# Optimization experiments

Hardware: AMD Instinct MI355X
Metric: run time of the kernel (lower is better)

## Reference

```python
import jax, jax.numpy as jnp
import numpy as np

B, D, H = 4096, 32, 1024  # batch, in_out_dim, hidden width


def setup_inputs() -> dict:
    key = jax.random.key(0)
    ks = jax.random.split(key, 10)

    def lin_w(k, shape, fan_in):
        bound = 1.0 / np.sqrt(fan_in)
        return jax.random.uniform(k, shape, jnp.float32, -bound, bound)

    return {
        "t": jax.random.uniform(ks[0], (1,), jnp.float32),
        "z": jax.random.normal(ks[1], (B, D), jnp.float32),
        "W0": lin_w(ks[2], (H, D + 1), D + 1),
        "b0": lin_w(ks[3], (H,), D + 1),
        "W1": lin_w(ks[4], (H, H), H),
        "b1": lin_w(ks[5], (H,), H),
        "W2": lin_w(ks[6], (H, H), H),
        "b2": lin_w(ks[7], (H,), H),
        "W3": lin_w(ks[8], (D, H), H),
        "b3": lin_w(ks[9], (D,), H),
    }


def _mlp(v, params):
    # Linear -> Tanh chain, final Linear (torch convention y = x @ W.T + b)
    for W, b in params[:-1]:
        v = jnp.tanh(v @ W.T + b)
    W, b = params[-1]
    return v @ W.T + b


def reference(t, z, W0, b0, W1, b1, W2, b2, W3, b3):
    bsz, d = z.shape
    tt = jnp.broadcast_to(t.reshape(-1), (bsz,))  # check_t: repeat scalar t
    params = [(W0, b0), (W1, b1), (W2, b2), (W3, b3)]

    def f(zz):  # [B, D] -> [B, D]
        v = jnp.concatenate([zz, tt[:, None]], axis=1)  # [B, D+1]
        return _mlp(v, params)

    out = f(z)

    # Exact Jacobian trace via d forward-mode JVPs (replaces the per-dim
    # autograd.grad loop in trace_df_dz with a single vmapped JVP batch).
    eye = jnp.eye(d, dtype=z.dtype)

    def jvp_i(e):
        return jax.jvp(f, (z,), (jnp.broadcast_to(e, z.shape),))[1]  # [B, D]

    tang = jax.vmap(jvp_i)(eye)            # [D, B, D]
    trace = jnp.einsum("ibi->b", tang)     # sum_i df_i/dz_i per sample
    divv = -trace
    return out, divv[:, None]
```

## Files before the change

kernel.cpp:

```cpp
#include <hip/hip_runtime.h>
#include <hip/hip_bf16.h>
#include <stdint.h>


using bf  = __hip_bfloat16;
using bf2 = __hip_bfloat162;
typedef __attribute__((ext_vector_type(8))) short bf16x8;
typedef __attribute__((ext_vector_type(4))) float f32x4;

__device__ __forceinline__ float b2f(bf x)    { return __bfloat162float(x); }
__device__ __forceinline__ bf    f2b(float x) { return __float2bfloat16(x); }

__global__ __launch_bounds__(256) void conv_k(const float* __restrict__ src,
                                              bf* __restrict__ dst, int n4) {
  const int i = blockIdx.x * 256 + threadIdx.x;
  if (i >= n4) return;
  float4 v = ((const float4*)src)[i];
  bf2* d = (bf2*)(dst + (size_t)i * 4);
  d[0] = __float22bfloat162_rn(make_float2(v.x, v.y));
  d[1] = __float22bfloat162_rn(make_float2(v.z, v.w));
}

__global__ void w0t_k(const float* __restrict__ W0, bf* __restrict__ W0T) {
  const int idx = blockIdx.x * 256 + threadIdx.x;
  const int i = idx >> 10, q = idx & 1023;
  W0T[idx] = f2b(W0[q * 33 + i]);
}

__global__ __launch_bounds__(256) void fwd0_k(const float* __restrict__ z,
                                              const float* __restrict__ tin,
                                              const float* __restrict__ W0,
                                              const float* __restrict__ b0,
                                              bf* __restrict__ h0) {
  __shared__ float zs[32 * 33];
  const int t = threadIdx.x;
  const int s0 = blockIdx.x * 32;
  for (int j = t; j < 1024; j += 256) {
    const int s = j >> 5, k = j & 31;
    zs[s * 33 + k] = z[(size_t)(s0 + s) * 32 + k];
  }
  if (t < 32) zs[t * 33 + 32] = tin[0];
  __syncthreads();
#pragma unroll 1
  for (int rep = 0; rep < 4; ++rep) {
    const int hh = rep * 256 + t;
    const float* wr = W0 + (size_t)hh * 33;
    float wv[33];
#pragma unroll
    for (int k = 0; k < 33; ++k) wv[k] = wr[k];
    const float bv = b0[hh];
#pragma unroll 1
    for (int s = 0; s < 32; ++s) {
      float acc = bv;
#pragma unroll
      for (int k = 0; k < 33; ++k) acc += wv[k] * zs[s * 33 + k];
      h0[(size_t)(s0 + s) * 1024 + hh] = f2b(tanhf(acc));
    }
  }
}

__global__ __launch_bounds__(256, 2) void gemm_fwd(const bf* __restrict__ A,
                                                   const bf* __restrict__ W,
                                                   const float* __restrict__ bias,
                                                   bf* __restrict__ H) {
  constexpr int K = 1024, N = 1024;
  __shared__ __align__(16) bf As[256 * 64];
  __shared__ __align__(16) bf Bs[128 * 64];
  const int t = threadIdx.x, l = t & 63, w = t >> 6;
  const int wm = w >> 1, wn = w & 1;
  const int f = blockIdx.x;
  const int n_t = (f >> 3) & 7, m_t = (f & 7) + 8 * (f >> 6);
  const size_t m0 = (size_t)m_t * 256, n0 = (size_t)n_t * 128;
  const int r15 = l & 15, q4 = l >> 4, sw = r15 & 7;

  const bf* asrc[8]; int aoff[8];
  const bf* bsrc[4]; int boff[4];
#pragma unroll
  for (int u = 0; u < 8; ++u) {
    const int sidx = u * 256 + t, row = sidx >> 3, seg = sidx & 7;
    asrc[u] = A + (m0 + row) * K + seg * 8;
    aoff[u] = row * 64 + ((seg ^ (row & 7)) * 8);
  }
#pragma unroll
  for (int u = 0; u < 4; ++u) {
    const int sidx = u * 256 + t, row = sidx >> 3, seg = sidx & 7;
    bsrc[u] = W + (n0 + row) * K + seg * 8;
    boff[u] = row * 64 + ((seg ^ (row & 7)) * 8);
  }

  f32x4 acc[8][4] = {};

  auto compute = [&]() {
#pragma unroll
    for (int kk = 0; kk < 2; ++kk) {
      const int sa = (kk * 4 + q4) ^ sw;
      bf16x8 af[8], bfr[4];
#pragma unroll
      for (int i = 0; i < 8; ++i)
        af[i] = *(const bf16x8*)(As + (wm * 128 + i * 16 + r15) * 64 + sa * 8);
#pragma unroll
      for (int j = 0; j < 4; ++j)
        bfr[j] = *(const bf16x8*)(Bs + (wn * 64 + j * 16 + r15) * 64 + sa * 8);
#pragma unroll
      for (int mi = 0; mi < 8; ++mi)
#pragma unroll
        for (int ni = 0; ni < 4; ++ni)
          acc[mi][ni] = __builtin_amdgcn_mfma_f32_16x16x32_bf16(af[mi], bfr[ni], acc[mi][ni], 0, 0, 0);
    }
  };

  {
    bf16x8 ra[8], rb[4];
#pragma unroll
    for (int u = 0; u < 8; ++u) ra[u] = *(const bf16x8*)(asrc[u]);
#pragma unroll
    for (int u = 0; u < 4; ++u) rb[u] = *(const bf16x8*)(bsrc[u]);
#pragma unroll
    for (int u = 0; u < 8; ++u) *(bf16x8*)(As + aoff[u]) = ra[u];
#pragma unroll
    for (int u = 0; u < 4; ++u) *(bf16x8*)(Bs + boff[u]) = rb[u];
  }
  __syncthreads();
#pragma unroll 1
  for (int k0 = 64; k0 < K; k0 += 64) {
    bf16x8 ra[8], rb[4];
#pragma unroll
    for (int u = 0; u < 8; ++u) ra[u] = *(const bf16x8*)(asrc[u] + k0);
#pragma unroll
    for (int u = 0; u < 4; ++u) rb[u] = *(const bf16x8*)(bsrc[u] + k0);
    compute();
    __syncthreads();
#pragma unroll
    for (int u = 0; u < 8; ++u) *(bf16x8*)(As + aoff[u]) = ra[u];
#pragma unroll
    for (int u = 0; u < 4; ++u) *(bf16x8*)(Bs + boff[u]) = rb[u];
    __syncthreads();
  }
  compute();

#pragma unroll
  for (int ni = 0; ni < 4; ++ni) {
    const int n = (int)n0 + wn * 64 + ni * 16 + r15;
    const float bv = bias[n];
#pragma unroll
    for (int mi = 0; mi < 8; ++mi)
#pragma unroll
      for (int r = 0; r < 4; ++r) {
        const size_t m = m0 + wm * 128 + mi * 16 + q4 * 4 + r;
        H[m * N + n] = f2b(tanhf(acc[mi][ni][r] + bv));
      }
  }
}

__global__ __launch_bounds__(256) void fwd3_k(const bf* __restrict__ h2,
                                              const bf* __restrict__ W3b,
                                              const float* __restrict__ b3,
                                              float* __restrict__ out) {
  __shared__ __align__(16) bf hs[8 * 1024];
  const int t = threadIdx.x;
  const size_t bb = (size_t)blockIdx.x * 8;
  const uint4* src = (const uint4*)(h2 + bb * 1024);
  uint4* dv = (uint4*)hs;
#pragma unroll
  for (int j = 0; j < 4; ++j) dv[j * 256 + t] = src[j * 256 + t];
  __syncthreads();
  const int i = t & 31, bl = t >> 5;
  const bf2* hr = (const bf2*)(hs + bl * 1024);
  const bf2* wr = (const bf2*)(W3b + (size_t)i * 1024);
  float s = 0.f;
#pragma unroll 8
  for (int k2 = 0; k2 < 512; ++k2) {
    float2 a = __bfloat1622float2(hr[k2]);
    float2 c = __bfloat1622float2(wr[k2]);
    s += a.x * c.x + a.y * c.y;
  }
  out[(bb + bl) * 32 + i] = s + b3[i];
}

__global__ __launch_bounds__(256) void t0_k(const bf* __restrict__ h0c,
                                            const bf* __restrict__ W0T,
                                            bf* __restrict__ T0) {
  const int idx = blockIdx.x * 256 + threadIdx.x;
  const int m = idx >> 6, seg = idx & 63;
  const int b = m >> 5, i = m & 31;
  const bf2* hp = (const bf2*)(h0c + (size_t)b * 1024 + seg * 16);
  const bf2* wp = (const bf2*)(W0T + (size_t)i * 1024 + seg * 16);
  bf2* dp = (bf2*)(T0 + (size_t)m * 1024 + seg * 16);
#pragma unroll
  for (int u = 0; u < 8; ++u) {
    float2 h = __bfloat1622float2(hp[u]);
    float2 w = __bfloat1622float2(wp[u]);
    float2 r;
    r.x = (1.f - h.x * h.x) * w.x;
    r.y = (1.f - h.y * h.y) * w.y;
    dp[u] = __float22bfloat162_rn(r);
  }
}

__global__ __launch_bounds__(256, 2) void gemm_jvp1(const bf* __restrict__ T0,
                                                    const bf* __restrict__ W1b,
                                                    const bf* __restrict__ h1c,
                                                    bf* __restrict__ T1) {
  constexpr int K = 1024, N = 1024;
  __shared__ __align__(16) bf As[256 * 64];
  __shared__ __align__(16) bf Bs[128 * 64];
  const int t = threadIdx.x, l = t & 63, w = t >> 6;
  const int wm = w >> 1, wn = w & 1;
  const int f = blockIdx.x;
  const int n_t = (f >> 3) & 7, m_t = (f & 7) + 8 * (f >> 6);
  const size_t m0 = (size_t)m_t * 256, n0 = (size_t)n_t * 128;
  const int r15 = l & 15, q4 = l >> 4, sw = r15 & 7;

  const bf* asrc[8]; int aoff[8];
  const bf* bsrc[4]; int boff[4];
#pragma unroll
  for (int u = 0; u < 8; ++u) {
    const int sidx = u * 256 + t, row = sidx >> 3, seg = sidx & 7;
    asrc[u] = T0 + (m0 + row) * K + seg * 8;
    aoff[u] = row * 64 + ((seg ^ (row & 7)) * 8);
  }
#pragma unroll
  for (int u = 0; u < 4; ++u) {
    const int sidx = u * 256 + t, row = sidx >> 3, seg = sidx & 7;
    bsrc[u] = W1b + (n0 + row) * K + seg * 8;
    boff[u] = row * 64 + ((seg ^ (row & 7)) * 8);
  }

  f32x4 acc[8][4] = {};

  auto compute = [&]() {
#pragma unroll
    for (int kk = 0; kk < 2; ++kk) {
      const int sa = (kk * 4 + q4) ^ sw;
      bf16x8 af[8], bfr[4];
#pragma unroll
      for (int i = 0; i < 8; ++i)
        af[i] = *(const bf16x8*)(As + (wm * 128 + i * 16 + r15) * 64 + sa * 8);
#pragma unroll
      for (int j = 0; j < 4; ++j)
        bfr[j] = *(const bf16x8*)(Bs + (wn * 64 + j * 16 + r15) * 64 + sa * 8);
#pragma unroll
      for (int mi = 0; mi < 8; ++mi)
#pragma unroll
        for (int ni = 0; ni < 4; ++ni)
          acc[mi][ni] = __builtin_amdgcn_mfma_f32_16x16x32_bf16(af[mi], bfr[ni], acc[mi][ni], 0, 0, 0);
    }
  };

  {
    bf16x8 ra[8], rb[4];
#pragma unroll
    for (int u = 0; u < 8; ++u) ra[u] = *(const bf16x8*)(asrc[u]);
#pragma unroll
    for (int u = 0; u < 4; ++u) rb[u] = *(const bf16x8*)(bsrc[u]);
#pragma unroll
    for (int u = 0; u < 8; ++u) *(bf16x8*)(As + aoff[u]) = ra[u];
#pragma unroll
    for (int u = 0; u < 4; ++u) *(bf16x8*)(Bs + boff[u]) = rb[u];
  }
  __syncthreads();
#pragma unroll 1
  for (int k0 = 64; k0 < K; k0 += 64) {
    bf16x8 ra[8], rb[4];
#pragma unroll
    for (int u = 0; u < 8; ++u) ra[u] = *(const bf16x8*)(asrc[u] + k0);
#pragma unroll
    for (int u = 0; u < 4; ++u) rb[u] = *(const bf16x8*)(bsrc[u] + k0);
    compute();
    __syncthreads();
#pragma unroll
    for (int u = 0; u < 8; ++u) *(bf16x8*)(As + aoff[u]) = ra[u];
#pragma unroll
    for (int u = 0; u < 4; ++u) *(bf16x8*)(Bs + boff[u]) = rb[u];
    __syncthreads();
  }
  compute();

  const int bbase = (int)((m0 + wm * 128) >> 5);
#pragma unroll
  for (int ni = 0; ni < 4; ++ni) {
    const int n = (int)n0 + wn * 64 + ni * 16 + r15;
    float a1v[4];
#pragma unroll
    for (int s = 0; s < 4; ++s) {
      const float hv = b2f(h1c[(size_t)(bbase + s) * 1024 + n]);
      a1v[s] = 1.f - hv * hv;
    }
#pragma unroll
    for (int mi = 0; mi < 8; ++mi)
#pragma unroll
      for (int r = 0; r < 4; ++r) {
        const size_t m = m0 + wm * 128 + mi * 16 + q4 * 4 + r;
        T1[m * N + n] = f2b(a1v[mi >> 1] * acc[mi][ni][r]);
      }
  }
}

__global__ __launch_bounds__(256, 2) void gemm_jvp2(const bf* __restrict__ T1,
                                                    const bf* __restrict__ W2b,
                                                    const bf* __restrict__ W3b,
                                                    const bf* __restrict__ h2c,
                                                    float* __restrict__ trace) {
  constexpr int K = 1024;
  __shared__ __align__(16) bf As[256 * 64];
  __shared__ __align__(16) bf Bs[128 * 64];
  const int t = threadIdx.x, l = t & 63, w = t >> 6;
  const int wm = w >> 1, wn = w & 1;
  const int f = blockIdx.x;
  const int n_t = (f >> 3) & 7, m_t = (f & 7) + 8 * (f >> 6);
  const size_t m0 = (size_t)m_t * 256, n0 = (size_t)n_t * 128;
  const int r15 = l & 15, q4 = l >> 4, sw = r15 & 7;

  const bf* asrc[8]; int aoff[8];
  const bf* bsrc[4]; int boff[4];
#pragma unroll
  for (int u = 0; u < 8; ++u) {
    const int sidx = u * 256 + t, row = sidx >> 3, seg = sidx & 7;
    asrc[u] = T1 + (m0 + row) * K + seg * 8;
    aoff[u] = row * 64 + ((seg ^ (row & 7)) * 8);
  }
#pragma unroll
  for (int u = 0; u < 4; ++u) {
    const int sidx = u * 256 + t, row = sidx >> 3, seg = sidx & 7;
    bsrc[u] = W2b + (n0 + row) * K + seg * 8;
    boff[u] = row * 64 + ((seg ^ (row & 7)) * 8);
  }

  f32x4 acc[8][4] = {};

  auto compute = [&]() {
#pragma unroll
    for (int kk = 0; kk < 2; ++kk) {
      const int sa = (kk * 4 + q4) ^ sw;
      bf16x8 af[8], bfr[4];
#pragma unroll
      for (int i = 0; i < 8; ++i)
        af[i] = *(const bf16x8*)(As + (wm * 128 + i * 16 + r15) * 64 + sa * 8);
#pragma unroll
      for (int j = 0; j < 4; ++j)
        bfr[j] = *(const bf16x8*)(Bs + (wn * 64 + j * 16 + r15) * 64 + sa * 8);
#pragma unroll
      for (int mi = 0; mi < 8; ++mi)
#pragma unroll
        for (int ni = 0; ni < 4; ++ni)
          acc[mi][ni] = __builtin_amdgcn_mfma_f32_16x16x32_bf16(af[mi], bfr[ni], acc[mi][ni], 0, 0, 0);
    }
  };

  {
    bf16x8 ra[8], rb[4];
#pragma unroll
    for (int u = 0; u < 8; ++u) ra[u] = *(const bf16x8*)(asrc[u]);
#pragma unroll
    for (int u = 0; u < 4; ++u) rb[u] = *(const bf16x8*)(bsrc[u]);
#pragma unroll
    for (int u = 0; u < 8; ++u) *(bf16x8*)(As + aoff[u]) = ra[u];
#pragma unroll
    for (int u = 0; u < 4; ++u) *(bf16x8*)(Bs + boff[u]) = rb[u];
  }
  __syncthreads();
#pragma unroll 1
  for (int k0 = 64; k0 < K; k0 += 64) {
    bf16x8 ra[8], rb[4];
#pragma unroll
    for (int u = 0; u < 8; ++u) ra[u] = *(const bf16x8*)(asrc[u] + k0);
#pragma unroll
    for (int u = 0; u < 4; ++u) rb[u] = *(const bf16x8*)(bsrc[u] + k0);
    compute();
    __syncthreads();
#pragma unroll
    for (int u = 0; u < 8; ++u) *(bf16x8*)(As + aoff[u]) = ra[u];
#pragma unroll
    for (int u = 0; u < 4; ++u) *(bf16x8*)(Bs + boff[u]) = rb[u];
    __syncthreads();
  }
  compute();

  const int bbase = (int)((m0 + wm * 128) >> 5);
  float part[4] = {0.f, 0.f, 0.f, 0.f};
#pragma unroll
  for (int ni = 0; ni < 4; ++ni) {
    const int n = (int)n0 + wn * 64 + ni * 16 + r15;
    float a2v[4];
#pragma unroll
    for (int s = 0; s < 4; ++s) {
      const float hv = b2f(h2c[(size_t)(bbase + s) * 1024 + n]);
      a2v[s] = 1.f - hv * hv;
    }
#pragma unroll
    for (int mi = 0; mi < 8; ++mi) {
      const int isel = mi >> 1;
#pragma unroll
      for (int r = 0; r < 4; ++r) {
        const int mm = wm * 128 + mi * 16 + q4 * 4 + r;
        part[isel] += b2f(W3b[(size_t)(mm & 31) * 1024 + n]) * a2v[isel] * acc[mi][ni][r];
      }
    }
  }
#pragma unroll
  for (int off = 32; off > 0; off >>= 1) {
#pragma unroll
    for (int s = 0; s < 4; ++s) part[s] += __shfl_down(part[s], off);
  }
  if (l == 0) {
#pragma unroll
    for (int s = 0; s < 4; ++s) atomicAdd(trace + bbase + s, -part[s]);
  }
}

__global__ void divv_k(const float* __restrict__ tr, float* __restrict__ dv) {
  const int b = blockIdx.x * 256 + threadIdx.x;
  dv[b] = tr[b];
}

extern "C" void kernel_launch(void* const* d_in, const int* in_sizes, int n_in,
                              void* d_out, int out_size, void* d_ws, size_t ws_size,
                              hipStream_t stream) {
  const float* tin = (const float*)d_in[0];
  const float* z   = (const float*)d_in[1];
  const float* W0  = (const float*)d_in[2];
  const float* b0  = (const float*)d_in[3];
  const float* W1  = (const float*)d_in[4];
  const float* b1  = (const float*)d_in[5];
  const float* W2  = (const float*)d_in[6];
  const float* b2  = (const float*)d_in[7];
  const float* W3  = (const float*)d_in[8];
  const float* b3  = (const float*)d_in[9];
  float* out = (float*)d_out;
  (void)in_sizes; (void)n_in; (void)out_size;

  char* ws = (char*)d_ws;
  size_t off = 0;
  auto take = [&](size_t bytes) {
    char* p = ws + off;
    off = (off + bytes + 255) & ~(size_t)255;
    return p;
  };
  bf* h0   = (bf*)take((size_t)4096 * 1024 * 2);
  bf* h1   = (bf*)take((size_t)4096 * 1024 * 2);
  bf* h2   = (bf*)take((size_t)4096 * 1024 * 2);
  bf* W0T  = (bf*)take((size_t)32 * 1024 * 2);
  bf* W1b  = (bf*)take((size_t)1024 * 1024 * 2);
  bf* W2b  = (bf*)take((size_t)1024 * 1024 * 2);
  bf* W3b  = (bf*)take((size_t)32 * 1024 * 2);
  float* tr = (float*)take((size_t)4096 * 4);
  const size_t avail = (ws_size > off) ? (ws_size - off) : 0;
  int NB = 4096;
  while (NB > 256 && 2 * (size_t)NB * 65536 > avail) NB >>= 1;
  bf* T0 = (bf*)take((size_t)NB * 65536);
  bf* T1 = (bf*)take((size_t)NB * 65536);

  hipMemsetAsync(tr, 0, 4096 * sizeof(float), stream);
  conv_k<<<dim3(1024), dim3(256), 0, stream>>>(W1, W1b, 262144);
  conv_k<<<dim3(1024), dim3(256), 0, stream>>>(W2, W2b, 262144);
  conv_k<<<dim3(32),   dim3(256), 0, stream>>>(W3, W3b, 8192);
  w0t_k<<<dim3(128), dim3(256), 0, stream>>>(W0, W0T);
  fwd0_k<<<dim3(128), dim3(256), 0, stream>>>(z, tin, W0, b0, h0);
  gemm_fwd<<<dim3(128), dim3(256), 0, stream>>>(h0, W1b, b1, h1);
  gemm_fwd<<<dim3(128), dim3(256), 0, stream>>>(h1, W2b, b2, h2);
  fwd3_k<<<dim3(512), dim3(256), 0, stream>>>(h2, W3b, b3, out);
  for (int cb = 0; cb < 4096; cb += NB) {
    t0_k<<<dim3(NB * 8), dim3(256), 0, stream>>>(h0 + (size_t)cb * 1024, W0T, T0);
    gemm_jvp1<<<dim3(NB), dim3(256), 0, stream>>>(
        T0, W1b, h1 + (size_t)cb * 1024, T1);
    gemm_jvp2<<<dim3(NB), dim3(256), 0, stream>>>(
        T1, W2b, W3b, h2 + (size_t)cb * 1024, tr + cb);
  }
  divv_k<<<dim3(16), dim3(256), 0, stream>>>(tr, out + 131072);
}
```

Before: 873.3 us.

## Merge independent kernels into shared launches to cut launch count and overlap work

Weight conversion, W0 transpose, the first layer and trace zeroing now run as one prep kernel, and the memset and divv copy kernel are gone because the atomic trace writes go straight to the output. The tangent T0 construction shares a launch with the first forward GEMM or the previous chunk's jvp2, and fwd3 shares a launch with jvp1. This cuts per-launch overhead and fills idle CUs during the small-grid GEMMs. The cost is larger register and shared-memory footprints on the light branches, which share the GEMM's launch bounds.

```diff
diff --git a/kernel.cpp b/kernel.cpp
--- a/kernel.cpp
+++ b/kernel.cpp
@@ -11,9 +11,9 @@
 __device__ __forceinline__ float b2f(bf x)    { return __bfloat162float(x); }
 __device__ __forceinline__ bf    f2b(float x) { return __float2bfloat16(x); }
 
-__global__ __launch_bounds__(256) void conv_k(const float* __restrict__ src,
-                                              bf* __restrict__ dst, int n4) {
-  const int i = blockIdx.x * 256 + threadIdx.x;
+__device__ __forceinline__ void conv_body(int blk, const float* __restrict__ src,
+                                          bf* __restrict__ dst, int n4) {
+  const int i = blk * 256 + threadIdx.x;
   if (i >= n4) return;
   float4 v = ((const float4*)src)[i];
   bf2* d = (bf2*)(dst + (size_t)i * 4);
@@ -21,56 +21,41 @@
   d[1] = __float22bfloat162_rn(make_float2(v.z, v.w));
 }
 
-__global__ void w0t_k(const float* __restrict__ W0, bf* __restrict__ W0T) {
-  const int idx = blockIdx.x * 256 + threadIdx.x;
+__device__ __forceinline__ void w0t_body(int blk, const float* __restrict__ W0,
+                                         bf* __restrict__ W0T) {
+  const int idx = blk * 256 + threadIdx.x;
   const int i = idx >> 10, q = idx & 1023;
   W0T[idx] = f2b(W0[q * 33 + i]);
 }
 
-__global__ __launch_bounds__(256) void fwd0_k(const float* __restrict__ z,
-                                              const float* __restrict__ tin,
-                                              const float* __restrict__ W0,
-                                              const float* __restrict__ b0,
-                                              bf* __restrict__ h0) {
-  __shared__ float zs[32 * 33];
-  const int t = threadIdx.x;
-  const int s0 = blockIdx.x * 32;
-  for (int j = t; j < 1024; j += 256) {
-    const int s = j >> 5, k = j & 31;
-    zs[s * 33 + k] = z[(size_t)(s0 + s) * 32 + k];
-  }
-  if (t < 32) zs[t * 33 + 32] = tin[0];
-  __syncthreads();
-#pragma unroll 1
-  for (int rep = 0; rep < 4; ++rep) {
-    const int hh = rep * 256 + t;
-    const float* wr = W0 + (size_t)hh * 33;
-    float wv[33];
-#pragma unroll
-    for (int k = 0; k < 33; ++k) wv[k] = wr[k];
-    const float bv = b0[hh];
-#pragma unroll 1
-    for (int s = 0; s < 32; ++s) {
-      float acc = bv;
-#pragma unroll
-      for (int k = 0; k < 33; ++k) acc += wv[k] * zs[s * 33 + k];
-      h0[(size_t)(s0 + s) * 1024 + hh] = f2b(tanhf(acc));
-    }
-  }
-}
-
-__global__ __launch_bounds__(256, 2) void gemm_fwd(const bf* __restrict__ A,
-                                                   const bf* __restrict__ W,
-                                                   const float* __restrict__ bias,
-                                                   bf* __restrict__ H) {
-  constexpr int K = 1024, N = 1024;
-  __shared__ __align__(16) bf As[256 * 64];
-  __shared__ __align__(16) bf Bs[128 * 64];
+__device__ __forceinline__ void t0_body(int blk, const bf* __restrict__ h0c,
+                                        const bf* __restrict__ W0T,
+                                        bf* __restrict__ T0) {
+  const int idx = blk * 256 + threadIdx.x;
+  const int m = idx >> 6, seg = idx & 63;
+  const int b = m >> 5, i = m & 31;
+  const bf2* hp = (const bf2*)(h0c + (size_t)b * 1024 + seg * 16);
+  const bf2* wp = (const bf2*)(W0T + (size_t)i * 1024 + seg * 16);
+  bf2* dp = (bf2*)(T0 + (size_t)m * 1024 + seg * 16);
+#pragma unroll
+  for (int u = 0; u < 8; ++u) {
+    float2 h = __bfloat1622float2(hp[u]);
+    float2 w = __bfloat1622float2(wp[u]);
+    float2 r;
+    r.x = (1.f - h.x * h.x) * w.x;
+    r.y = (1.f - h.y * h.y) * w.y;
+    dp[u] = __float22bfloat162_rn(r);
+  }
+}
+
+__device__ __forceinline__ void gemm_core(bf* As, bf* Bs,
+                                          const bf* __restrict__ A,
+                                          const bf* __restrict__ B,
+                                          size_t m0, size_t n0,
+                                          f32x4 (&acc)[8][4]) {
+  constexpr int K = 1024;
   const int t = threadIdx.x, l = t & 63, w = t >> 6;
   const int wm = w >> 1, wn = w & 1;
-  const int f = blockIdx.x;
-  const int n_t = (f >> 3) & 7, m_t = (f & 7) + 8 * (f >> 6);
-  const size_t m0 = (size_t)m_t * 256, n0 = (size_t)n_t * 128;
   const int r15 = l & 15, q4 = l >> 4, sw = r15 & 7;
 
   const bf* asrc[8]; int aoff[8];
@@ -84,11 +69,9 @@
 #pragma unroll
   for (int u = 0; u < 4; ++u) {
     const int sidx = u * 256 + t, row = sidx >> 3, seg = sidx & 7;
-    bsrc[u] = W + (n0 + row) * K + seg * 8;
+    bsrc[u] = B + (n0 + row) * K + seg * 8;
     boff[u] = row * 64 + ((seg ^ (row & 7)) * 8);
   }
-
-  f32x4 acc[8][4] = {};
 
   auto compute = [&]() {
 #pragma unroll
@@ -137,28 +120,15 @@
     __syncthreads();
   }
   compute();
-
-#pragma unroll
-  for (int ni = 0; ni < 4; ++ni) {
-    const int n = (int)n0 + wn * 64 + ni * 16 + r15;
-    const float bv = bias[n];
-#pragma unroll
-    for (int mi = 0; mi < 8; ++mi)
-#pragma unroll
-      for (int r = 0; r < 4; ++r) {
-        const size_t m = m0 + wm * 128 + mi * 16 + q4 * 4 + r;
-        H[m * N + n] = f2b(tanhf(acc[mi][ni][r] + bv));
-      }
-  }
-}
-
-__global__ __launch_bounds__(256) void fwd3_k(const bf* __restrict__ h2,
-                                              const bf* __restrict__ W3b,
-                                              const float* __restrict__ b3,
-                                              float* __restrict__ out) {
-  __shared__ __align__(16) bf hs[8 * 1024];
+}
+
+__device__ __forceinline__ void fwd3_body(bf* hs, int blk,
+                                          const bf* __restrict__ h2,
+                                          const bf* __restrict__ W3b,
+                                          const float* __restrict__ b3,
+                                          float* __restrict__ out) {
   const int t = threadIdx.x;
-  const size_t bb = (size_t)blockIdx.x * 8;
+  const size_t bb = (size_t)blk * 8;
   const uint4* src = (const uint4*)(h2 + bb * 1024);
   uint4* dv = (uint4*)hs;
 #pragma unroll
@@ -177,105 +147,111 @@
   out[(bb + bl) * 32 + i] = s + b3[i];
 }
 
-__global__ __launch_bounds__(256) void t0_k(const bf* __restrict__ h0c,
-                                            const bf* __restrict__ W0T,
-                                            bf* __restrict__ T0) {
-  const int idx = blockIdx.x * 256 + threadIdx.x;
-  const int m = idx >> 6, seg = idx & 63;
-  const int b = m >> 5, i = m & 31;
-  const bf2* hp = (const bf2*)(h0c + (size_t)b * 1024 + seg * 16);
-  const bf2* wp = (const bf2*)(W0T + (size_t)i * 1024 + seg * 16);
-  bf2* dp = (bf2*)(T0 + (size_t)m * 1024 + seg * 16);
-#pragma unroll
-  for (int u = 0; u < 8; ++u) {
-    float2 h = __bfloat1622float2(hp[u]);
-    float2 w = __bfloat1622float2(wp[u]);
-    float2 r;
-    r.x = (1.f - h.x * h.x) * w.x;
-    r.y = (1.f - h.y * h.y) * w.y;
-    dp[u] = __float22bfloat162_rn(r);
-  }
-}
-
-__global__ __launch_bounds__(256, 2) void gemm_jvp1(const bf* __restrict__ T0,
-                                                    const bf* __restrict__ W1b,
-                                                    const bf* __restrict__ h1c,
-                                                    bf* __restrict__ T1) {
-  constexpr int K = 1024, N = 1024;
-  __shared__ __align__(16) bf As[256 * 64];
-  __shared__ __align__(16) bf Bs[128 * 64];
+__global__ __launch_bounds__(256) void prep_k(const float* __restrict__ z,
+                                              const float* __restrict__ tin,
+                                              const float* __restrict__ W0,
+                                              const float* __restrict__ b0,
+                                              const float* __restrict__ W1,
+                                              const float* __restrict__ W2,
+                                              const float* __restrict__ W3,
+                                              bf* __restrict__ h0,
+                                              bf* __restrict__ W0T,
+                                              bf* __restrict__ W1b,
+                                              bf* __restrict__ W2b,
+                                              bf* __restrict__ W3b,
+                                              float* __restrict__ out2) {
+  __shared__ float zs[32 * 33];
+  const int f = blockIdx.x, t = threadIdx.x;
+  if (f < 128) {
+    const int s0 = f * 32;
+    for (int j = t; j < 1024; j += 256) {
+      const int s = j >> 5, k = j & 31;
+      zs[s * 33 + k] = z[(size_t)(s0 + s) * 32 + k];
+    }
+    if (t < 32) zs[t * 33 + 32] = tin[0];
+    __syncthreads();
+#pragma unroll 1
+    for (int rep = 0; rep < 4; ++rep) {
+      const int hh = rep * 256 + t;
+      const float* wr = W0 + (size_t)hh * 33;
+      float wv[33];
+#pragma unroll
+      for (int k = 0; k < 33; ++k) wv[k] = wr[k];
+      const float bv = b0[hh];
+#pragma unroll 1
+      for (int s = 0; s < 32; ++s) {
+        float acc = bv;
+#pragma unroll
+        for (int k = 0; k < 33; ++k) acc += wv[k] * zs[s * 33 + k];
+        h0[(size_t)(s0 + s) * 1024 + hh] = f2b(tanhf(acc));
+      }
+    }
+  } else if (f < 1152) {
+    conv_body(f - 128, W1, W1b, 262144);
+  } else if (f < 2176) {
+    conv_body(f - 1152, W2, W2b, 262144);
+  } else if (f < 2208) {
+    conv_body(f - 2176, W3, W3b, 8192);
+  } else if (f < 2336) {
+    w0t_body(f - 2208, W0, W0T);
+  } else {
+#pragma unroll
+    for (int u = 0; u < 16; ++u) out2[u * 256 + t] = 0.f;
+  }
+}
+
+__global__ __launch_bounds__(256, 2) void fwd_t0_k(const bf* __restrict__ A,
+                                                   const bf* __restrict__ W,
+                                                   const float* __restrict__ bias,
+                                                   bf* __restrict__ H,
+                                                   const bf* __restrict__ h0c,
+                                                   const bf* __restrict__ W0T,
+                                                   bf* __restrict__ T0) {
+  __shared__ __align__(16) bf smem[24576];
+  const int f = blockIdx.x;
+  if (f >= 128) { t0_body(f - 128, h0c, W0T, T0); return; }
+  constexpr int N = 1024;
   const int t = threadIdx.x, l = t & 63, w = t >> 6;
   const int wm = w >> 1, wn = w & 1;
-  const int f = blockIdx.x;
   const int n_t = (f >> 3) & 7, m_t = (f & 7) + 8 * (f >> 6);
   const size_t m0 = (size_t)m_t * 256, n0 = (size_t)n_t * 128;
-  const int r15 = l & 15, q4 = l >> 4, sw = r15 & 7;
-
-  const bf* asrc[8]; int aoff[8];
-  const bf* bsrc[4]; int boff[4];
-#pragma unroll
-  for (int u = 0; u < 8; ++u) {
-    const int sidx = u * 256 + t, row = sidx >> 3, seg = sidx & 7;
-    asrc[u] = T0 + (m0 + row) * K + seg * 8;
-    aoff[u] = row * 64 + ((seg ^ (row & 7)) * 8);
-  }
-#pragma unroll
-  for (int u = 0; u < 4; ++u) {
-    const int sidx = u * 256 + t, row = sidx >> 3, seg = sidx & 7;
-    bsrc[u] = W1b + (n0 + row) * K + seg * 8;
-    boff[u] = row * 64 + ((seg ^ (row & 7)) * 8);
-  }
-
+  const int r15 = l & 15, q4 = l >> 4;
   f32x4 acc[8][4] = {};
-
-  auto compute = [&]() {
-#pragma unroll
-    for (int kk = 0; kk < 2; ++kk) {
-      const int sa = (kk * 4 + q4) ^ sw;
-      bf16x8 af[8], bfr[4];
-#pragma unroll
-      for (int i = 0; i < 8; ++i)
-        af[i] = *(const bf16x8*)(As + (wm * 128 + i * 16 + r15) * 64 + sa * 8);
-#pragma unroll
-      for (int j = 0; j < 4; ++j)
-        bfr[j] = *(const bf16x8*)(Bs + (wn * 64 + j * 16 + r15) * 64 + sa * 8);
-#pragma unroll
-      for (int mi = 0; mi < 8; ++mi)
-#pragma unroll
-        for (int ni = 0; ni < 4; ++ni)
-          acc[mi][ni] = __builtin_amdgcn_mfma_f32_16x16x32_bf16(af[mi], bfr[ni], acc[mi][ni], 0, 0, 0);
-    }
-  };
-
-  {
-    bf16x8 ra[8], rb[4];
-#pragma unroll
-    for (int u = 0; u < 8; ++u) ra[u] = *(const bf16x8*)(asrc[u]);
-#pragma unroll
-    for (int u = 0; u < 4; ++u) rb[u] = *(const bf16x8*)(bsrc[u]);
-#pragma unroll
-    for (int u = 0; u < 8; ++u) *(bf16x8*)(As + aoff[u]) = ra[u];
-#pragma unroll
-    for (int u = 0; u < 4; ++u) *(bf16x8*)(Bs + boff[u]) = rb[u];
-  }
-  __syncthreads();
-#pragma unroll 1
-  for (int k0 = 64; k0 < K; k0 += 64) {
-    bf16x8 ra[8], rb[4];
-#pragma unroll
-    for (int u = 0; u < 8; ++u) ra[u] = *(const bf16x8*)(asrc[u] + k0);
-#pragma unroll
-    for (int u = 0; u < 4; ++u) rb[u] = *(const bf16x8*)(bsrc[u] + k0);
-    compute();
-    __syncthreads();
-#pragma unroll
-    for (int u = 0; u < 8; ++u) *(bf16x8*)(As + aoff[u]) = ra[u];
-#pragma unroll
-    for (int u = 0; u < 4; ++u) *(bf16x8*)(Bs + boff[u]) = rb[u];
-    __syncthreads();
-  }
-  compute();
-
+  gemm_core(smem, smem + 16384, A, W, m0, n0, acc);
+#pragma unroll
+  for (int ni = 0; ni < 4; ++ni) {
+    const int n = (int)n0 + wn * 64 + ni * 16 + r15;
+    const float bv = bias[n];
+#pragma unroll
+    for (int mi = 0; mi < 8; ++mi)
+#pragma unroll
+      for (int r = 0; r < 4; ++r) {
+        const size_t m = m0 + wm * 128 + mi * 16 + q4 * 4 + r;
+        H[m * N + n] = f2b(tanhf(acc[mi][ni][r] + bv));
+      }
+  }
+}
+
+__global__ __launch_bounds__(256, 2) void jvp1_fwd3_k(const bf* __restrict__ T0,
+                                                      const bf* __restrict__ W1b,
+                                                      const bf* __restrict__ h1c,
+                                                      bf* __restrict__ T1,
+                                                      const bf* __restrict__ h2,
+                                                      const bf* __restrict__ W3b,
+                                                      const float* __restrict__ b3,
+                                                      float* __restrict__ out,
+                                                      int njvp) {
+  __shared__ __align__(16) bf smem[24576];
+  const int f = blockIdx.x;
+  if (f >= njvp) { fwd3_body(smem, f - njvp, h2, W3b, b3, out); return; }
+  constexpr int N = 1024;
+  const int t = threadIdx.x, l = t & 63, w = t >> 6;
+  const int wm = w >> 1, wn = w & 1;
+  const int n_t = (f >> 3) & 7, m_t = (f & 7) + 8 * (f >> 6);
+  const size_t m0 = (size_t)m_t * 256, n0 = (size_t)n_t * 128;
+  const int r15 = l & 15, q4 = l >> 4;
+  f32x4 acc[8][4] = {};
+  gemm_core(smem, smem + 16384, T0, W1b, m0, n0, acc);
   const int bbase = (int)((m0 + wm * 128) >> 5);
 #pragma unroll
   for (int ni = 0; ni < 4; ++ni) {
@@ -296,86 +272,25 @@
   }
 }
 
-__global__ __launch_bounds__(256, 2) void gemm_jvp2(const bf* __restrict__ T1,
+__global__ __launch_bounds__(256, 2) void jvp2_t0_k(const bf* __restrict__ T1,
                                                     const bf* __restrict__ W2b,
                                                     const bf* __restrict__ W3b,
                                                     const bf* __restrict__ h2c,
-                                                    float* __restrict__ trace) {
-  constexpr int K = 1024;
-  __shared__ __align__(16) bf As[256 * 64];
-  __shared__ __align__(16) bf Bs[128 * 64];
+                                                    float* __restrict__ out2c,
+                                                    const bf* __restrict__ h0n,
+                                                    const bf* __restrict__ W0T,
+                                                    bf* __restrict__ T0,
+                                                    int njvp) {
+  __shared__ __align__(16) bf smem[24576];
+  const int f = blockIdx.x;
+  if (f >= njvp) { t0_body(f - njvp, h0n, W0T, T0); return; }
   const int t = threadIdx.x, l = t & 63, w = t >> 6;
   const int wm = w >> 1, wn = w & 1;
-  const int f = blockIdx.x;
   const int n_t = (f >> 3) & 7, m_t = (f & 7) + 8 * (f >> 6);
   const size_t m0 = (size_t)m_t * 256, n0 = (size_t)n_t * 128;
-  const int r15 = l & 15, q4 = l >> 4, sw = r15 & 7;
-
-  const bf* asrc[8]; int aoff[8];
-  const bf* bsrc[4]; int boff[4];
-#pragma unroll
-  for (int u = 0; u < 8; ++u) {
-    const int sidx = u * 256 + t, row = sidx >> 3, seg = sidx & 7;
-    asrc[u] = T1 + (m0 + row) * K + seg * 8;
-    aoff[u] = row * 64 + ((seg ^ (row & 7)) * 8);
-  }
-#pragma unroll
-  for (int u = 0; u < 4; ++u) {
-    const int sidx = u * 256 + t, row = sidx >> 3, seg = sidx & 7;
-    bsrc[u] = W2b + (n0 + row) * K + seg * 8;
-    boff[u] = row * 64 + ((seg ^ (row & 7)) * 8);
-  }
-
+  const int r15 = l & 15, q4 = l >> 4;
   f32x4 acc[8][4] = {};
-
-  auto compute = [&]() {
-#pragma unroll
-    for (int kk = 0; kk < 2; ++kk) {
-      const int sa = (kk * 4 + q4) ^ sw;
-      bf16x8 af[8], bfr[4];
-#pragma unroll
-      for (int i = 0; i < 8; ++i)
-        af[i] = *(const bf16x8*)(As + (wm * 128 + i * 16 + r15) * 64 + sa * 8);
-#pragma unroll
-      for (int j = 0; j < 4; ++j)
-        bfr[j] = *(const bf16x8*)(Bs + (wn * 64 + j * 16 + r15) * 64 + sa * 8);
-#pragma unroll
-      for (int mi = 0; mi < 8; ++mi)
-#pragma unroll
-        for (int ni = 0; ni < 4; ++ni)
-          acc[mi][ni] = __builtin_amdgcn_mfma_f32_16x16x32_bf16(af[mi], bfr[ni], acc[mi][ni], 0, 0, 0);
-    }
-  };
-
-  {
-    bf16x8 ra[8], rb[4];
-#pragma unroll
-    for (int u = 0; u < 8; ++u) ra[u] = *(const bf16x8*)(asrc[u]);
-#pragma unroll
-    for (int u = 0; u < 4; ++u) rb[u] = *(const bf16x8*)(bsrc[u]);
-#pragma unroll
-    for (int u = 0; u < 8; ++u) *(bf16x8*)(As + aoff[u]) = ra[u];
-#pragma unroll
-    for (int u = 0; u < 4; ++u) *(bf16x8*)(Bs + boff[u]) = rb[u];
-  }
-  __syncthreads();
-#pragma unroll 1
-  for (int k0 = 64; k0 < K; k0 += 64) {
-    bf16x8 ra[8], rb[4];
-#pragma unroll
-    for (int u = 0; u < 8; ++u) ra[u] = *(const bf16x8*)(asrc[u] + k0);
-#pragma unroll
-    for (int u = 0; u < 4; ++u) rb[u] = *(const bf16x8*)(bsrc[u] + k0);
-    compute();
-    __syncthreads();
-#pragma unroll
-    for (int u = 0; u < 8; ++u) *(bf16x8*)(As + aoff[u]) = ra[u];
-#pragma unroll
-    for (int u = 0; u < 4; ++u) *(bf16x8*)(Bs + boff[u]) = rb[u];
-    __syncthreads();
-  }
-  compute();
-
+  gemm_core(smem, smem + 16384, T1, W2b, m0, n0, acc);
   const int bbase = (int)((m0 + wm * 128) >> 5);
   float part[4] = {0.f, 0.f, 0.f, 0.f};
 #pragma unroll
@@ -404,13 +319,8 @@
   }
   if (l == 0) {
 #pragma unroll
-    for (int s = 0; s < 4; ++s) atomicAdd(trace + bbase + s, -part[s]);
-  }
-}
-
-__global__ void divv_k(const float* __restrict__ tr, float* __restrict__ dv) {
-  const int b = blockIdx.x * 256 + threadIdx.x;
-  dv[b] = tr[b];
+    for (int s = 0; s < 4; ++s) atomicAdd(out2c + bbase + s, -part[s]);
+  }
 }
 
 extern "C" void kernel_launch(void* const* d_in, const int* in_sizes, int n_in,
@@ -427,6 +337,7 @@
   const float* W3  = (const float*)d_in[8];
   const float* b3  = (const float*)d_in[9];
   float* out = (float*)d_out;
+  float* out2 = out + 131072;
   (void)in_sizes; (void)n_in; (void)out_size;
 
   char* ws = (char*)d_ws;
@@ -443,28 +354,31 @@
   bf* W1b  = (bf*)take((size_t)1024 * 1024 * 2);
   bf* W2b  = (bf*)take((size_t)1024 * 1024 * 2);
   bf* W3b  = (bf*)take((size_t)32 * 1024 * 2);
-  float* tr = (float*)take((size_t)4096 * 4);
   const size_t avail = (ws_size > off) ? (ws_size - off) : 0;
   int NB = 4096;
   while (NB > 256 && 2 * (size_t)NB * 65536 > avail) NB >>= 1;
   bf* T0 = (bf*)take((size_t)NB * 65536);
   bf* T1 = (bf*)take((size_t)NB * 65536);
 
-  hipMemsetAsync(tr, 0, 4096 * sizeof(float), stream);
-  conv_k<<<dim3(1024), dim3(256), 0, stream>>>(W1, W1b, 262144);
-  conv_k<<<dim3(1024), dim3(256), 0, stream>>>(W2, W2b, 262144);
-  conv_k<<<dim3(32),   dim3(256), 0, stream>>>(W3, W3b, 8192);
-  w0t_k<<<dim3(128), dim3(256), 0, stream>>>(W0, W0T);
-  fwd0_k<<<dim3(128), dim3(256), 0, stream>>>(z, tin, W0, b0, h0);
-  gemm_fwd<<<dim3(128), dim3(256), 0, stream>>>(h0, W1b, b1, h1);
-  gemm_fwd<<<dim3(128), dim3(256), 0, stream>>>(h1, W2b, b2, h2);
-  fwd3_k<<<dim3(512), dim3(256), 0, stream>>>(h2, W3b, b3, out);
-  for (int cb = 0; cb < 4096; cb += NB) {
-    t0_k<<<dim3(NB * 8), dim3(256), 0, stream>>>(h0 + (size_t)cb * 1024, W0T, T0);
-    gemm_jvp1<<<dim3(NB), dim3(256), 0, stream>>>(
-        T0, W1b, h1 + (size_t)cb * 1024, T1);
-    gemm_jvp2<<<dim3(NB), dim3(256), 0, stream>>>(
-        T1, W2b, W3b, h2 + (size_t)cb * 1024, tr + cb);
-  }
-  divv_k<<<dim3(16), dim3(256), 0, stream>>>(tr, out + 131072);
-}
+  prep_k<<<dim3(2337), dim3(256), 0, stream>>>(z, tin, W0, b0, W1, W2, W3,
+                                               h0, W0T, W1b, W2b, W3b, out2);
+  fwd_t0_k<<<dim3(128 + NB * 8), dim3(256), 0, stream>>>(h0, W1b, b1, h1,
+                                                         h0, W0T, T0);
+  fwd_t0_k<<<dim3(128), dim3(256), 0, stream>>>(h1, W2b, b2, h2, h0, W0T, T0);
+  const int nchunk = 4096 / NB;
+  for (int c = 0; c < nchunk; ++c) {
+    const int cb = c * NB;
+    const int g1 = (c == 0) ? NB + 512 : NB;
+    jvp1_fwd3_k<<<dim3(g1), dim3(256), 0, stream>>>(
+        T0, W1b, h1 + (size_t)cb * 1024, T1, h2, W3b, b3, out, NB);
+    if (c + 1 < nchunk) {
+      jvp2_t0_k<<<dim3(NB + NB * 8), dim3(256), 0, stream>>>(
+          T1, W2b, W3b, h2 + (size_t)cb * 1024, out2 + cb,
+          h0 + (size_t)(cb + NB) * 1024, W0T, T0, NB);
+    } else {
+      jvp2_t0_k<<<dim3(NB), dim3(256), 0, stream>>>(
+          T1, W2b, W3b, h2 + (size_t)cb * 1024, out2 + cb,
+          h0, W0T, T0, NB);
+    }
+  }
+}
```

New measurement: 855.0 us. -2.1%, faster.
